# Optimization experiments

Measured on AMD Instinct MI355X. Metric: run time of the kernel, lower is better.

Reference implementation:

```python
import jax, jax.numpy as jnp
import numpy as np

B, T, N, F = 1, 12, 20000, 1
E = 320000
D, H, NH = 64, 64, 4


def setup_inputs() -> dict:
    ki = iter(jax.random.split(jax.random.key(0), 64))

    def rn(shape, s=0.05):
        return jax.random.normal(next(ki), shape, jnp.float32) * s

    z = lambda *s: jnp.zeros(s, jnp.float32)
    o = lambda *s: jnp.ones(s, jnp.float32)
    inp = {}
    inp['x_seq'] = jax.random.normal(next(ki), (B, T, N, F), jnp.float32)
    inp['edge_index'] = jax.random.randint(next(ki), (2, E), 0, N)
    inp['edge_weight'] = jax.random.uniform(next(ki), (E,), jnp.float32)
    inp['Wpi'] = rn((F, D)); inp['bpi'] = z(D)
    for nm, shp in [('Wq', (D, D)), ('Wk', (D, D)), ('Wv', (D, D)), ('Wo', (D, D)), ('W1', (D, 4 * D)), ('W2', (4 * D, D)), ('Wpo', (D, F))]:
        inp[nm] = rn(shp)
    for nm, d in [('bq', D), ('bk', D), ('bv', D), ('bo', D), ('b1', 4 * D), ('b2', D), ('bpo', F)]:
        inp[nm] = z(d)
    inp['g1'] = o(D); inp['be1'] = z(D); inp['g2'] = o(D); inp['be2'] = z(D)
    # GConvGRU gate params: A* (x self), B* (x neighbor), C*/D* (h self/neighbor)
    for a, bn, bb, c, d, cb in [('Az', 'Bz', 'bz', 'Cz', 'Dz', 'cz'), ('Ar', 'Br', 'br', 'Cr', 'Dr', 'cr'), ('Ah', 'Bh', 'bg', 'Ch', 'Dh', 'cg')]:
        inp[a] = rn((F, H)); inp[bn] = rn((F, H)); inp[bb] = z(H)
        inp[c] = rn((H, H)); inp[d] = rn((H, H)); inp[cb] = z(H)
    inp['Whd'] = rn((H, 1)); inp['bhd'] = z(1)
    return inp


def reference(x_seq, edge_index, edge_weight, Wpi, bpi, Wq, bq, Wk, bk, Wv, bv, Wo, bo, g1, be1, W1, b1, W2, b2, g2, be2, Wpo, bpo, Az, Bz, bz, Cz, Dz, cz, Ar, Br, br, Cr, Dr, cr, Ah, Bh, bg, Ch, Dh, cg, Whd, bhd):
    B_, T_, N_, F_ = x_seq.shape
    M = B_ * N_
    dh = D // NH

    def ln(y, g, b):
        m = y.mean(-1, keepdims=True)
        v = ((y - m) ** 2).mean(-1, keepdims=True)
        return (y - m) / jnp.sqrt(v + 1e-5) * g + b

    # per-node temporal Transformer (post-LN, relu FFN, dropout=eval)
    x = x_seq.transpose(0, 2, 1, 3).reshape(M, T_, F_)  # [M,T,F]
    x = x @ Wpi + bpi  # [M,T,D]
    q = (x @ Wq + bq).reshape(M, T_, NH, dh)
    k = (x @ Wk + bk).reshape(M, T_, NH, dh)
    v = (x @ Wv + bv).reshape(M, T_, NH, dh)
    att = jax.nn.softmax(jnp.einsum('mqhd,mkhd->mhqk', q, k) / jnp.sqrt(jnp.float32(dh)), axis=-1)
    a = jnp.einsum('mhqk,mkhd->mqhd', att, v).reshape(M, T_, D) @ Wo + bo
    x = ln(x + a, g1, be1)
    f = jax.nn.relu(x @ W1 + b1) @ W2 + b2
    x = ln(x + f, g2, be2)
    x = x @ Wpo + bpo  # [M,T,F]
    xs = x.reshape(B_, N_, T_, F_).transpose(2, 0, 1, 3)  # [T,B,N,F]

    src, dst = edge_index[0], edge_index[1]
    ew = edge_weight[None, :, None]

    def gconv(y, Ws, Wn, b):
        msg = jnp.zeros_like(y).at[:, dst].add(y[:, src] * ew)
        return y @ Ws + msg @ Wn + b

    def step(h, xt):
        zt = jax.nn.sigmoid(gconv(xt, Az, Bz, bz) + gconv(h, Cz, Dz, cz))
        rt = jax.nn.sigmoid(gconv(xt, Ar, Br, br) + gconv(h, Cr, Dr, cr))
        gt = jnp.tanh(gconv(xt, Ah, Bh, bg) + gconv(rt * h, Ch, Dh, cg))
        h = zt * h + (1.0 - zt) * gt
        return h, None

    h0 = jnp.zeros((B_, N_, H), x_seq.dtype)
    h, _ = jax.lax.scan(step, h0, xs)
    return jax.nn.relu(h) @ Whd + bhd  # [B,N,1]
```

## Files before the change

kernel.cpp:

```cpp
#include <hip/hip_runtime.h>
#include <math.h>

#define TT 12
#define NN 20000
#define EE 320000

__device__ __forceinline__ float wsum64(float v) {
#pragma unroll
    for (int o = 32; o >= 1; o >>= 1) v += __shfl_xor(v, o);
    return v;
}

__device__ __forceinline__ float wsum16(float v) {
#pragma unroll
    for (int o = 8; o >= 1; o >>= 1) v += __shfl_xor(v, o);
    return v;
}

__device__ __forceinline__ float rdlane(float v, int l) {
    return __int_as_float(__builtin_amdgcn_readlane(__float_as_int(v), l));
}

__global__ void k_precomp(const float* __restrict__ Wpi, const float* __restrict__ bpi,
                          const float* __restrict__ Wq, const float* __restrict__ bq,
                          const float* __restrict__ Wk, const float* __restrict__ bk,
                          const float* __restrict__ Wv, const float* __restrict__ bv,
                          const float* __restrict__ Wo, const float* __restrict__ bo,
                          const float* __restrict__ g1, const float* __restrict__ be1,
                          const float* __restrict__ W1, const float* __restrict__ b1,
                          float* __restrict__ PC) {
    __shared__ float sWq[64], sWk[64], sWv[64], sBq[64], sBk[64], sBv[64];
    const int tid = threadIdx.x;
    if (tid < 64) {
        int d = tid;
        float wq = 0, wk = 0, wv = 0, vbq = 0, vbk = 0, vbv = 0;
        for (int e = 0; e < 64; ++e) {
            float wp = Wpi[e], bp = bpi[e];
            wq = fmaf(wp, Wq[e * 64 + d], wq);
            wk = fmaf(wp, Wk[e * 64 + d], wk);
            wv = fmaf(wp, Wv[e * 64 + d], wv);
            vbq = fmaf(bp, Wq[e * 64 + d], vbq);
            vbk = fmaf(bp, Wk[e * 64 + d], vbk);
            vbv = fmaf(bp, Wv[e * 64 + d], vbv);
        }
        sWq[d] = wq; sWk[d] = wk; sWv[d] = wv;
        sBq[d] = vbq + bq[d]; sBk[d] = vbk + bk[d]; sBv[d] = vbv + bv[d];
    }
    __syncthreads();
    if (tid < 16) {
        int h = tid >> 2, which = tid & 3;
        float s = 0;
        for (int j = 0; j < 16; ++j) {
            int e = h * 16 + j;
            float a = (which < 2) ? sWq[e] : sBq[e];
            float b = (which & 1) ? sBk[e] : sWk[e];
            s = fmaf(a, b, s);
        }
        PC[320 + which * 4 + h] = s;
    }
    {
        int h = tid >> 6, d = tid & 63;
        float s = 0;
        for (int j = 0; j < 16; ++j) {
            int e = h * 16 + j;
            s = fmaf(sWv[e], Wo[e * 64 + d], s);
        }
        PC[h * 64 + d] = s;
    }
    if (tid < 64) {
        int d = tid;
        float s = 0;
        for (int e = 0; e < 64; ++e) s = fmaf(sBv[e], Wo[e * 64 + d], s);
        PC[256 + d] = s + bo[d] + bpi[d];
    }
    __syncthreads();
    {
        int k = tid;
        for (int r = 0; r < 8; ++r) {
            float s = (r == 7) ? b1[k] : 0.0f;
            for (int d = 0; d < 64; ++d) {
                float b;
                if (r == 0) b = Wpi[d] * g1[d];
                else if (r < 5) b = PC[(r - 1) * 64 + d] * g1[d];
                else if (r == 5) b = PC[256 + d] * g1[d];
                else if (r == 6) b = g1[d];
                else b = be1[d];
                s = fmaf(b, W1[d * 256 + k], s);
            }
            PC[384 + r * 256 + k] = s;
        }
    }
}

__global__ void k_zero_offs(int* __restrict__ offs) {
    int i = blockIdx.x * 256 + threadIdx.x;
    if (i < NN + 1) offs[i] = 0;
}
__global__ void k_count(const int* __restrict__ dst, int* __restrict__ offs) {
    int e = blockIdx.x * 256 + threadIdx.x;
    if (e < EE) atomicAdd(&offs[dst[e] + 1], 1);
}
__global__ void k_scan(int* __restrict__ offs, int* __restrict__ cur) {
    __shared__ int buf[1024];
    __shared__ int carry;
    int tid = threadIdx.x;
    if (tid == 0) carry = 0;
    __syncthreads();
    const int total = NN + 1;
    for (int base = 0; base < total; base += 1024) {
        int idx = base + tid;
        int v = (idx < total) ? offs[idx] : 0;
        buf[tid] = v;
        __syncthreads();
        for (int o = 1; o < 1024; o <<= 1) {
            int t = (tid >= o) ? buf[tid - o] : 0;
            __syncthreads();
            buf[tid] += t;
            __syncthreads();
        }
        int incl = buf[tid] + carry;
        if (idx < total) offs[idx] = incl;
        __syncthreads();
        if (tid == 1023) carry += buf[1023];
        __syncthreads();
    }
    for (int i = tid; i < NN; i += 1024) cur[i] = offs[i];
}
__global__ void k_fill(const int* __restrict__ src, const int* __restrict__ dst,
                       const float* __restrict__ w, int* __restrict__ cur,
                       int2* __restrict__ ep) {
    int e = blockIdx.x * 256 + threadIdx.x;
    if (e < EE) {
        int dn = dst[e];
        int slot = atomicAdd(&cur[dn], 1);
        ep[slot] = make_int2(src[e], __float_as_int(w[e]));
    }
}

__global__ void __launch_bounds__(256)
k_transformer(const float* __restrict__ x_seq,
              const float* __restrict__ Wpi,
              const float* __restrict__ g1, const float* __restrict__ be1,
              const float* __restrict__ b2,
              const float* __restrict__ g2, const float* __restrict__ be2,
              const float* __restrict__ W2,
              const float* __restrict__ PC,
              const float* __restrict__ Wpo, const float* __restrict__ bpo,
              float* __restrict__ XS) {
    __shared__ __align__(16) float sCV[4][TT][4];
    __shared__ __align__(16) float sRelu[4][TT][64];
    __shared__ __align__(16) float sX1[4][TT][64];
    __shared__ float sIvsv[4][TT];
    __shared__ float sMiv[4][TT];
    const int wid = threadIdx.x >> 6;
    const int d = threadIdx.x & 63;
    const int n = blockIdx.x * 4 + wid;

    float sv[TT];
#pragma unroll
    for (int t = 0; t < TT; ++t) sv[t] = x_seq[t * NN + n];

    {
        const int hh = d >> 4;
        const int qi = d & 15;
        const float alpha = PC[320 + hh], beta = PC[324 + hh];
        const float gamma = PC[328 + hh], delta = PC[332 + hh];
        if (qi < TT) {
            float si = sv[qi];
            float a1 = 0.25f * fmaf(si, alpha, gamma);
            float a0 = 0.25f * fmaf(si, beta, delta);
            float sc[TT];
            float mx = -1e30f;
#pragma unroll
            for (int j = 0; j < TT; ++j) {
                sc[j] = fmaf(sv[j], a1, a0);
                mx = fmaxf(mx, sc[j]);
            }
            float ssum = 0.f;
#pragma unroll
            for (int j = 0; j < TT; ++j) { sc[j] = __expf(sc[j] - mx); ssum += sc[j]; }
            float inv = 1.0f / ssum;
            float cv = 0.f;
#pragma unroll
            for (int j = 0; j < TT; ++j) cv = fmaf(sc[j] * inv, sv[j], cv);
            sCV[wid][qi][hh] = cv;
        }
    }
    __syncthreads();

    float ivv[TT];
    const float inv64 = 1.0f / 64.0f;
    {
        const float u = Wpi[d];
        const float g1d = g1[d], be1d = be1[d];
        const float vo0 = PC[d], vo1 = PC[64 + d], vo2 = PC[128 + d], vo3 = PC[192 + d];
        const float c0 = PC[256 + d];
#pragma unroll
        for (int t = 0; t < TT; ++t) {
            float4 cv4 = *(const float4*)(&sCV[wid][t][0]);
            float y = fmaf(sv[t], u, c0);
            y = fmaf(cv4.x, vo0, y); y = fmaf(cv4.y, vo1, y);
            y = fmaf(cv4.z, vo2, y); y = fmaf(cv4.w, vo3, y);
            float s1 = wsum64(y);
            float s2 = wsum64(y * y);
            float m = s1 * inv64;
            float var = s2 * inv64 - m * m;
            float iv = rsqrtf(var + 1e-5f);
            ivv[t] = iv;
            sX1[wid][t][d] = (y - m) * iv * g1d + be1d;
            if (d == 0) {
                sIvsv[wid][t] = sv[t] * iv;
                sMiv[wid][t] = -m * iv;
            }
        }
    }

    float y2[TT];
    {
        float b2d = b2[d];
#pragma unroll
        for (int t = 0; t < TT; ++t) y2[t] = b2d;
    }
#pragma unroll
    for (int kk = 0; kk < 4; ++kk) {
        const float* P = PC + 384 + kk * 64 + d;
        float P0 = P[0], P1 = P[256], P2 = P[512], P3 = P[768];
        float P4 = P[1024], P5 = P[1280], P6 = P[1536], P7 = P[1792];
#pragma unroll
        for (int t = 0; t < TT; ++t) {
            float4 cv4 = *(const float4*)(&sCV[wid][t][0]);
            float iv = ivv[t];
            float hp = P7;
            hp = fmaf(sIvsv[wid][t], P0, hp);
            hp = fmaf(cv4.x * iv, P1, hp);
            hp = fmaf(cv4.y * iv, P2, hp);
            hp = fmaf(cv4.z * iv, P3, hp);
            hp = fmaf(cv4.w * iv, P4, hp);
            hp = fmaf(iv, P5, hp);
            hp = fmaf(sMiv[wid][t], P6, hp);
            sRelu[wid][t][d] = fmaxf(hp, 0.0f);
        }
#pragma unroll 4
        for (int kg = 0; kg < 64; kg += 4) {
            const float* wb = W2 + (kk * 64 + kg) * 64 + d;
            float w0 = wb[0], w1 = wb[64], w2 = wb[128], w3 = wb[192];
#pragma unroll
            for (int t = 0; t < TT; ++t) {
                float4 rv = *(const float4*)(&sRelu[wid][t][kg]);
                y2[t] = fmaf(rv.x, w0, fmaf(rv.y, w1, fmaf(rv.z, w2, fmaf(rv.w, w3, y2[t]))));
            }
        }
    }

    {
        float g2d = g2[d], be2d = be2[d], wpod = Wpo[d];
        float bpo0 = bpo[0];
#pragma unroll
        for (int t = 0; t < TT; ++t) {
            float y = sX1[wid][t][d] + y2[t];
            float s1 = wsum64(y);
            float s2 = wsum64(y * y);
            float m = s1 * inv64;
            float var = s2 * inv64 - m * m;
            float iv = rsqrtf(var + 1e-5f);
            float x2 = (y - m) * iv * g2d + be2d;
            float p = wsum64(x2 * wpod);
            if (d == 0) XS[n * TT + t] = p + bpo0;
        }
    }
}

__global__ void k_gather_x(const float* __restrict__ XS,
                           const int* __restrict__ offs, const int2* __restrict__ ep,
                           float* __restrict__ MX) {
    const int wid = threadIdx.x >> 6;
    const int lane = threadIdx.x & 63;
    const int lg = lane >> 4;
    const int el = lane & 15;
    const int n = (blockIdx.x * 4 + wid) * 4 + lg;
    int beg = offs[n], end = offs[n + 1];
    float4 a0 = {0,0,0,0}, a1 = {0,0,0,0}, a2 = {0,0,0,0};
    for (int i = beg + el; i < end; i += 16) {
        int2 e = ep[i];
        float w = __int_as_float(e.y);
        const float4* xr = (const float4*)(XS + (size_t)e.x * TT);
        float4 v0 = xr[0], v1 = xr[1], v2 = xr[2];
        a0.x = fmaf(w, v0.x, a0.x); a0.y = fmaf(w, v0.y, a0.y);
        a0.z = fmaf(w, v0.z, a0.z); a0.w = fmaf(w, v0.w, a0.w);
        a1.x = fmaf(w, v1.x, a1.x); a1.y = fmaf(w, v1.y, a1.y);
        a1.z = fmaf(w, v1.z, a1.z); a1.w = fmaf(w, v1.w, a1.w);
        a2.x = fmaf(w, v2.x, a2.x); a2.y = fmaf(w, v2.y, a2.y);
        a2.z = fmaf(w, v2.z, a2.z); a2.w = fmaf(w, v2.w, a2.w);
    }
    float acc[TT] = { a0.x, a0.y, a0.z, a0.w, a1.x, a1.y, a1.z, a1.w,
                      a2.x, a2.y, a2.z, a2.w };
#pragma unroll
    for (int t = 0; t < TT; ++t) acc[t] = wsum16(acc[t]);
    if (el == 0) {
#pragma unroll
        for (int t = 0; t < TT; ++t) MX[n * TT + t] = acc[t];
    }
}

__global__ void k_gather_vec(const float* __restrict__ V,
                             const int* __restrict__ offs, const int2* __restrict__ ep,
                             float* __restrict__ out) {
    const int wid = threadIdx.x >> 6;
    const int d = threadIdx.x & 63;
    const int n = blockIdx.x * 4 + wid;
    int beg = offs[n], end = offs[n + 1];
    float m0 = 0, m1 = 0, m2 = 0, m3 = 0, m4 = 0, m5 = 0, m6 = 0, m7 = 0;
    int i = beg;
    for (; i + 8 <= end; i += 8) {
        int2 e0 = ep[i], e1 = ep[i+1], e2 = ep[i+2], e3 = ep[i+3];
        int2 e4 = ep[i+4], e5 = ep[i+5], e6 = ep[i+6], e7 = ep[i+7];
        m0 = fmaf(__int_as_float(e0.y), V[(size_t)e0.x * 64 + d], m0);
        m1 = fmaf(__int_as_float(e1.y), V[(size_t)e1.x * 64 + d], m1);
        m2 = fmaf(__int_as_float(e2.y), V[(size_t)e2.x * 64 + d], m2);
        m3 = fmaf(__int_as_float(e3.y), V[(size_t)e3.x * 64 + d], m3);
        m4 = fmaf(__int_as_float(e4.y), V[(size_t)e4.x * 64 + d], m4);
        m5 = fmaf(__int_as_float(e5.y), V[(size_t)e5.x * 64 + d], m5);
        m6 = fmaf(__int_as_float(e6.y), V[(size_t)e6.x * 64 + d], m6);
        m7 = fmaf(__int_as_float(e7.y), V[(size_t)e7.x * 64 + d], m7);
    }
    for (; i < end; ++i) {
        int2 e = ep[i];
        m0 = fmaf(__int_as_float(e.y), V[(size_t)e.x * 64 + d], m0);
    }
    out[(size_t)n * 64 + d] = ((m0 + m1) + (m2 + m3)) + ((m4 + m5) + (m6 + m7));
}

__global__ void k_gates_a(const float* __restrict__ XS, const float* __restrict__ MX, int tstep,
                          const float* __restrict__ h, const float* __restrict__ MH,
                          const float* __restrict__ Az, const float* __restrict__ Bz,
                          const float* __restrict__ bz,
                          const float* __restrict__ Cz, const float* __restrict__ Dz,
                          const float* __restrict__ cz,
                          const float* __restrict__ Ar, const float* __restrict__ Br,
                          const float* __restrict__ br,
                          const float* __restrict__ Cr, const float* __restrict__ Dr,
                          const float* __restrict__ cr,
                          float* __restrict__ zb, float* __restrict__ rh) {
    const int wid = threadIdx.x >> 6;
    const int d = threadIdx.x & 63;
    const int nb = (blockIdx.x * 4 + wid) * 8;

    float hreg[8], mreg[8], zacc[8], racc[8];
    {
        float azd = Az[d], bzd = Bz[d], cz0 = bz[d] + cz[d];
        float ard = Ar[d], brd = Br[d], cr0 = br[d] + cr[d];
#pragma unroll
        for (int g = 0; g < 8; ++g) {
            int n = nb + g;
            hreg[g] = h[(size_t)n * 64 + d];
            mreg[g] = MH[(size_t)n * 64 + d];
            float xt = XS[n * TT + tstep];
            float mx = MX[n * TT + tstep];
            zacc[g] = fmaf(xt, azd, fmaf(mx, bzd, cz0));
            racc[g] = fmaf(xt, ard, fmaf(mx, brd, cr0));
        }
    }
#pragma unroll 4
    for (int k = 0; k < 64; ++k) {
        float wcz = Cz[k * 64 + d], wdz = Dz[k * 64 + d];
        float wcr = Cr[k * 64 + d], wdr = Dr[k * 64 + d];
#pragma unroll
        for (int g = 0; g < 8; ++g) {
            float hk = rdlane(hreg[g], k);
            float mk = rdlane(mreg[g], k);
            zacc[g] = fmaf(hk, wcz, fmaf(mk, wdz, zacc[g]));
            racc[g] = fmaf(hk, wcr, fmaf(mk, wdr, racc[g]));
        }
    }
#pragma unroll
    for (int g = 0; g < 8; ++g) {
        int n = nb + g;
        float z = 1.0f / (1.0f + __expf(-zacc[g]));
        float r = 1.0f / (1.0f + __expf(-racc[g]));
        zb[(size_t)n * 64 + d] = z;
        rh[(size_t)n * 64 + d] = r * hreg[g];
    }
}

__global__ void k_gates_b(const float* __restrict__ XS, const float* __restrict__ MX, int tstep,
                          float* __restrict__ h,
                          const float* __restrict__ zb, const float* __restrict__ rh,
                          const float* __restrict__ MRH,
                          const float* __restrict__ Ah, const float* __restrict__ Bh,
                          const float* __restrict__ bg,
                          const float* __restrict__ Ch, const float* __restrict__ Dh,
                          const float* __restrict__ cg,
                          const float* __restrict__ Whd, const float* __restrict__ bhd,
                          float* __restrict__ out, int last) {
    const int wid = threadIdx.x >> 6;
    const int d = threadIdx.x & 63;
    const int nb = (blockIdx.x * 4 + wid) * 8;

    float rreg[8], mreg[8], gacc[8];
    {
        float ahd = Ah[d], bhd_ = Bh[d], cg0 = bg[d] + cg[d];
#pragma unroll
        for (int g = 0; g < 8; ++g) {
            int n = nb + g;
            rreg[g] = rh[(size_t)n * 64 + d];
            mreg[g] = MRH[(size_t)n * 64 + d];
            float xt = XS[n * TT + tstep];
            float mx = MX[n * TT + tstep];
            gacc[g] = fmaf(xt, ahd, fmaf(mx, bhd_, cg0));
        }
    }
#pragma unroll 4
    for (int k = 0; k < 64; ++k) {
        float wch = Ch[k * 64 + d], wdh = Dh[k * 64 + d];
#pragma unroll
        for (int g = 0; g < 8; ++g) {
            float rk = rdlane(rreg[g], k);
            float mk = rdlane(mreg[g], k);
            gacc[g] = fmaf(rk, wch, fmaf(mk, wdh, gacc[g]));
        }
    }
#pragma unroll
    for (int g = 0; g < 8; ++g) {
        int n = nb + g;
        float gg = tanhf(gacc[g]);
        float z = zb[(size_t)n * 64 + d];
        float hold = h[(size_t)n * 64 + d];
        float hnew = z * hold + (1.0f - z) * gg;
        h[(size_t)n * 64 + d] = hnew;
        if (last) {
            float p = fmaxf(hnew, 0.0f) * Whd[d];
            float s = wsum64(p);
            if (d == 0) out[n] = s + bhd[0];
        }
    }
}

extern "C" void kernel_launch(void* const* d_in, const int* in_sizes, int n_in,
                              void* d_out, int out_size, void* d_ws, size_t ws_size,
                              hipStream_t stream) {
    const float* x_seq = (const float*)d_in[0];
    const int* eidx = (const int*)d_in[1];
    const float* ew = (const float*)d_in[2];
    const float* Wpi = (const float*)d_in[3];
    const float* bpi = (const float*)d_in[4];
    const float* Wq = (const float*)d_in[5];
    const float* Wk = (const float*)d_in[6];
    const float* Wv = (const float*)d_in[7];
    const float* Wo = (const float*)d_in[8];
    const float* W1 = (const float*)d_in[9];
    const float* W2 = (const float*)d_in[10];
    const float* Wpo = (const float*)d_in[11];
    const float* bq = (const float*)d_in[12];
    const float* bk = (const float*)d_in[13];
    const float* bv = (const float*)d_in[14];
    const float* bo = (const float*)d_in[15];
    const float* b1 = (const float*)d_in[16];
    const float* b2 = (const float*)d_in[17];
    const float* bpo = (const float*)d_in[18];
    const float* g1 = (const float*)d_in[19];
    const float* be1 = (const float*)d_in[20];
    const float* g2 = (const float*)d_in[21];
    const float* be2 = (const float*)d_in[22];
    const float* Az = (const float*)d_in[23];
    const float* Bz = (const float*)d_in[24];
    const float* bz = (const float*)d_in[25];
    const float* Cz = (const float*)d_in[26];
    const float* Dz = (const float*)d_in[27];
    const float* cz = (const float*)d_in[28];
    const float* Ar = (const float*)d_in[29];
    const float* Br = (const float*)d_in[30];
    const float* br_ = (const float*)d_in[31];
    const float* Cr = (const float*)d_in[32];
    const float* Dr = (const float*)d_in[33];
    const float* cr_ = (const float*)d_in[34];
    const float* Ah = (const float*)d_in[35];
    const float* Bh = (const float*)d_in[36];
    const float* bg = (const float*)d_in[37];
    const float* Ch = (const float*)d_in[38];
    const float* Dh = (const float*)d_in[39];
    const float* cg = (const float*)d_in[40];
    const float* Whd = (const float*)d_in[41];
    const float* bhd = (const float*)d_in[42];

    float* ws = (float*)d_ws;
    float* XS = ws;
    float* hbuf = XS + 240000;
    float* rhbuf = hbuf + 1280000;
    float* zbuf = rhbuf + 1280000;
    float* msg = zbuf + 1280000;
    float* PC = msg + 1280000;
    int* ioffs = (int*)(PC + 2560);
    int* cur = ioffs + (NN + 1);
    int2* ep = (int2*)(cur + NN + 1);
    float* MX = (float*)(ep + EE);

    const int* e_src = eidx;
    const int* e_dst = eidx + EE;

    hipMemsetAsync(hbuf, 0, (size_t)NN * 64 * sizeof(float), stream);
    k_precomp<<<1, 256, 0, stream>>>(Wpi, bpi, Wq, bq, Wk, bk, Wv, bv, Wo, bo,
                                     g1, be1, W1, b1, PC);
    k_zero_offs<<<(NN + 1 + 255) / 256, 256, 0, stream>>>(ioffs);
    k_count<<<(EE + 255) / 256, 256, 0, stream>>>(e_dst, ioffs);
    k_scan<<<1, 1024, 0, stream>>>(ioffs, cur);
    k_fill<<<(EE + 255) / 256, 256, 0, stream>>>(e_src, e_dst, ew, cur, ep);

    k_transformer<<<5000, 256, 0, stream>>>(x_seq, Wpi, g1, be1, b2, g2, be2,
                                            W2, PC, Wpo, bpo, XS);

    k_gather_x<<<1250, 256, 0, stream>>>(XS, ioffs, ep, MX);

    for (int t = 0; t < TT; ++t) {
        k_gather_vec<<<5000, 256, 0, stream>>>(hbuf, ioffs, ep, msg);
        k_gates_a<<<625, 256, 0, stream>>>(XS, MX, t, hbuf, msg,
                                           Az, Bz, bz, Cz, Dz, cz,
                                           Ar, Br, br_, Cr, Dr, cr_,
                                           zbuf, rhbuf);
        k_gather_vec<<<5000, 256, 0, stream>>>(rhbuf, ioffs, ep, msg);
        k_gates_b<<<625, 256, 0, stream>>>(XS, MX, t, hbuf, zbuf, rhbuf, msg,
                                           Ah, Bh, bg, Ch, Dh, cg,
                                           Whd, bhd, (float*)d_out, (t == TT - 1) ? 1 : 0);
    }
}
```

Before: 1.376 ms.

## Fuse GRU time loop into one cooperative kernel; keep FFN hidden in registers

The 48 per-timestep launches of the GRU recurrence are replaced by a single persistent cooperative kernel. It runs the gather and gate phases with grid-wide syncs between them, with the multi-launch path kept as a fallback. Separately, the transformer FFN now holds the ReLU hidden activations in registers and broadcasts them with readlane instead of staging them in shared memory. The aim is to remove launch overhead and shared-memory traffic. The trade-offs are grid.sync cost, a grid size limited by occupancy, and higher register pressure in the transformer (launch bounds set to 1).

```diff
diff --git a/kernel.cpp b/kernel.cpp
--- a/kernel.cpp
+++ b/kernel.cpp
@@ -1,5 +1,8 @@
 #include <hip/hip_runtime.h>
+#include <hip/hip_cooperative_groups.h>
 #include <math.h>
+
+namespace cg = cooperative_groups;
 
 #define TT 12
 #define NN 20000
@@ -137,7 +140,7 @@
     }
 }
 
-__global__ void __launch_bounds__(256)
+__global__ void __launch_bounds__(256, 1)
 k_transformer(const float* __restrict__ x_seq,
               const float* __restrict__ Wpi,
               const float* __restrict__ g1, const float* __restrict__ be1,
@@ -148,7 +151,6 @@
               const float* __restrict__ Wpo, const float* __restrict__ bpo,
               float* __restrict__ XS) {
     __shared__ __align__(16) float sCV[4][TT][4];
-    __shared__ __align__(16) float sRelu[4][TT][64];
     __shared__ __align__(16) float sX1[4][TT][64];
     __shared__ float sIvsv[4][TT];
     __shared__ float sMiv[4][TT];
@@ -214,41 +216,51 @@
             }
         }
     }
-
-    float y2[TT];
-    {
-        float b2d = b2[d];
-#pragma unroll
-        for (int t = 0; t < TT; ++t) y2[t] = b2d;
-    }
-#pragma unroll
-    for (int kk = 0; kk < 4; ++kk) {
-        const float* P = PC + 384 + kk * 64 + d;
-        float P0 = P[0], P1 = P[256], P2 = P[512], P3 = P[768];
-        float P4 = P[1024], P5 = P[1280], P6 = P[1536], P7 = P[1792];
+    __syncthreads();
+
+    float hpreg[TT][4];
+    {
+        float Pr[8][4];
+#pragma unroll
+        for (int r = 0; r < 8; ++r)
+#pragma unroll
+            for (int kk = 0; kk < 4; ++kk)
+                Pr[r][kk] = PC[384 + r * 256 + kk * 64 + d];
 #pragma unroll
         for (int t = 0; t < TT; ++t) {
             float4 cv4 = *(const float4*)(&sCV[wid][t][0]);
             float iv = ivv[t];
-            float hp = P7;
-            hp = fmaf(sIvsv[wid][t], P0, hp);
-            hp = fmaf(cv4.x * iv, P1, hp);
-            hp = fmaf(cv4.y * iv, P2, hp);
-            hp = fmaf(cv4.z * iv, P3, hp);
-            hp = fmaf(cv4.w * iv, P4, hp);
-            hp = fmaf(iv, P5, hp);
-            hp = fmaf(sMiv[wid][t], P6, hp);
-            sRelu[wid][t][d] = fmaxf(hp, 0.0f);
-        }
+            float civ = sIvsv[wid][t];
+            float cmv = sMiv[wid][t];
+#pragma unroll
+            for (int kk = 0; kk < 4; ++kk) {
+                float hp = Pr[7][kk];
+                hp = fmaf(civ, Pr[0][kk], hp);
+                hp = fmaf(cv4.x * iv, Pr[1][kk], hp);
+                hp = fmaf(cv4.y * iv, Pr[2][kk], hp);
+                hp = fmaf(cv4.z * iv, Pr[3][kk], hp);
+                hp = fmaf(cv4.w * iv, Pr[4][kk], hp);
+                hp = fmaf(iv, Pr[5][kk], hp);
+                hp = fmaf(cmv, Pr[6][kk], hp);
+                hpreg[t][kk] = fmaxf(hp, 0.0f);
+            }
+        }
+    }
+
+    float y2[TT];
+    {
+        float b2d = b2[d];
+#pragma unroll
+        for (int t = 0; t < TT; ++t) y2[t] = b2d;
+    }
+#pragma unroll
+    for (int kk = 0; kk < 4; ++kk) {
 #pragma unroll 4
-        for (int kg = 0; kg < 64; kg += 4) {
-            const float* wb = W2 + (kk * 64 + kg) * 64 + d;
-            float w0 = wb[0], w1 = wb[64], w2 = wb[128], w3 = wb[192];
-#pragma unroll
-            for (int t = 0; t < TT; ++t) {
-                float4 rv = *(const float4*)(&sRelu[wid][t][kg]);
-                y2[t] = fmaf(rv.x, w0, fmaf(rv.y, w1, fmaf(rv.z, w2, fmaf(rv.w, w3, y2[t]))));
-            }
+        for (int kin = 0; kin < 64; ++kin) {
+            float w = W2[(kk * 64 + kin) * 64 + d];
+#pragma unroll
+            for (int t = 0; t < TT; ++t)
+                y2[t] = fmaf(rdlane(hpreg[t][kk], kin), w, y2[t]);
         }
     }
 
@@ -432,6 +444,164 @@
             float s = wsum64(p);
             if (d == 0) out[n] = s + bhd[0];
         }
+    }
+}
+
+__global__ void __launch_bounds__(256, 4)
+k_gru_coop(const float* __restrict__ XS, const float* __restrict__ MX,
+           float* __restrict__ h, float* __restrict__ zb, float* __restrict__ rh,
+           float* __restrict__ msg,
+           const int* __restrict__ offs, const int2* __restrict__ ep,
+           const float* __restrict__ Az, const float* __restrict__ Bz,
+           const float* __restrict__ bz,
+           const float* __restrict__ Cz, const float* __restrict__ Dz,
+           const float* __restrict__ cz,
+           const float* __restrict__ Ar, const float* __restrict__ Br,
+           const float* __restrict__ br,
+           const float* __restrict__ Cr, const float* __restrict__ Dr,
+           const float* __restrict__ cr,
+           const float* __restrict__ Ah, const float* __restrict__ Bh,
+           const float* __restrict__ bg,
+           const float* __restrict__ Ch, const float* __restrict__ Dh,
+           const float* __restrict__ cg,
+           const float* __restrict__ Whd, const float* __restrict__ bhd,
+           float* __restrict__ out) {
+    cg::grid_group grid = cg::this_grid();
+    const int wid = threadIdx.x >> 6;
+    const int d = threadIdx.x & 63;
+    const int gw = blockIdx.x * 4 + wid;
+    const int NW = gridDim.x * 4;
+
+    for (int t = 0; t < TT; ++t) {
+        for (int n = gw; n < NN; n += NW) {
+            int beg = offs[n], end = offs[n + 1];
+            float m0 = 0, m1 = 0, m2 = 0, m3 = 0, m4 = 0, m5 = 0, m6 = 0, m7 = 0;
+            int i = beg;
+            for (; i + 8 <= end; i += 8) {
+                int2 e0 = ep[i], e1 = ep[i+1], e2 = ep[i+2], e3 = ep[i+3];
+                int2 e4 = ep[i+4], e5 = ep[i+5], e6 = ep[i+6], e7 = ep[i+7];
+                m0 = fmaf(__int_as_float(e0.y), h[(size_t)e0.x * 64 + d], m0);
+                m1 = fmaf(__int_as_float(e1.y), h[(size_t)e1.x * 64 + d], m1);
+                m2 = fmaf(__int_as_float(e2.y), h[(size_t)e2.x * 64 + d], m2);
+                m3 = fmaf(__int_as_float(e3.y), h[(size_t)e3.x * 64 + d], m3);
+                m4 = fmaf(__int_as_float(e4.y), h[(size_t)e4.x * 64 + d], m4);
+                m5 = fmaf(__int_as_float(e5.y), h[(size_t)e5.x * 64 + d], m5);
+                m6 = fmaf(__int_as_float(e6.y), h[(size_t)e6.x * 64 + d], m6);
+                m7 = fmaf(__int_as_float(e7.y), h[(size_t)e7.x * 64 + d], m7);
+            }
+            for (; i < end; ++i) {
+                int2 e = ep[i];
+                m0 = fmaf(__int_as_float(e.y), h[(size_t)e.x * 64 + d], m0);
+            }
+            msg[(size_t)n * 64 + d] = ((m0 + m1) + (m2 + m3)) + ((m4 + m5) + (m6 + m7));
+        }
+        grid.sync();
+
+        for (int task = gw; task < NN / 8; task += NW) {
+            const int nb = task * 8;
+            float hreg[8], mreg[8], zacc[8], racc[8];
+            {
+                float azd = Az[d], bzd = Bz[d], cz0 = bz[d] + cz[d];
+                float ard = Ar[d], brd = Br[d], cr0 = br[d] + cr[d];
+#pragma unroll
+                for (int g = 0; g < 8; ++g) {
+                    int n = nb + g;
+                    hreg[g] = h[(size_t)n * 64 + d];
+                    mreg[g] = msg[(size_t)n * 64 + d];
+                    float xt = XS[n * TT + t];
+                    float mx = MX[n * TT + t];
+                    zacc[g] = fmaf(xt, azd, fmaf(mx, bzd, cz0));
+                    racc[g] = fmaf(xt, ard, fmaf(mx, brd, cr0));
+                }
+            }
+#pragma unroll 4
+            for (int k = 0; k < 64; ++k) {
+                float wcz = Cz[k * 64 + d], wdz = Dz[k * 64 + d];
+                float wcr = Cr[k * 64 + d], wdr = Dr[k * 64 + d];
+#pragma unroll
+                for (int g = 0; g < 8; ++g) {
+                    float hk = rdlane(hreg[g], k);
+                    float mk = rdlane(mreg[g], k);
+                    zacc[g] = fmaf(hk, wcz, fmaf(mk, wdz, zacc[g]));
+                    racc[g] = fmaf(hk, wcr, fmaf(mk, wdr, racc[g]));
+                }
+            }
+#pragma unroll
+            for (int g = 0; g < 8; ++g) {
+                int n = nb + g;
+                float z = 1.0f / (1.0f + __expf(-zacc[g]));
+                float r = 1.0f / (1.0f + __expf(-racc[g]));
+                zb[(size_t)n * 64 + d] = z;
+                rh[(size_t)n * 64 + d] = r * hreg[g];
+            }
+        }
+        grid.sync();
+
+        for (int n = gw; n < NN; n += NW) {
+            int beg = offs[n], end = offs[n + 1];
+            float m0 = 0, m1 = 0, m2 = 0, m3 = 0, m4 = 0, m5 = 0, m6 = 0, m7 = 0;
+            int i = beg;
+            for (; i + 8 <= end; i += 8) {
+                int2 e0 = ep[i], e1 = ep[i+1], e2 = ep[i+2], e3 = ep[i+3];
+                int2 e4 = ep[i+4], e5 = ep[i+5], e6 = ep[i+6], e7 = ep[i+7];
+                m0 = fmaf(__int_as_float(e0.y), rh[(size_t)e0.x * 64 + d], m0);
+                m1 = fmaf(__int_as_float(e1.y), rh[(size_t)e1.x * 64 + d], m1);
+                m2 = fmaf(__int_as_float(e2.y), rh[(size_t)e2.x * 64 + d], m2);
+                m3 = fmaf(__int_as_float(e3.y), rh[(size_t)e3.x * 64 + d], m3);
+                m4 = fmaf(__int_as_float(e4.y), rh[(size_t)e4.x * 64 + d], m4);
+                m5 = fmaf(__int_as_float(e5.y), rh[(size_t)e5.x * 64 + d], m5);
+                m6 = fmaf(__int_as_float(e6.y), rh[(size_t)e6.x * 64 + d], m6);
+                m7 = fmaf(__int_as_float(e7.y), rh[(size_t)e7.x * 64 + d], m7);
+            }
+            for (; i < end; ++i) {
+                int2 e = ep[i];
+                m0 = fmaf(__int_as_float(e.y), rh[(size_t)e.x * 64 + d], m0);
+            }
+            msg[(size_t)n * 64 + d] = ((m0 + m1) + (m2 + m3)) + ((m4 + m5) + (m6 + m7));
+        }
+        grid.sync();
+
+        for (int task = gw; task < NN / 8; task += NW) {
+            const int nb = task * 8;
+            float rreg[8], mreg[8], gacc[8];
+            {
+                float ahd = Ah[d], bhd_ = Bh[d], cg0 = bg[d] + cg[d];
+#pragma unroll
+                for (int g = 0; g < 8; ++g) {
+                    int n = nb + g;
+                    rreg[g] = rh[(size_t)n * 64 + d];
+                    mreg[g] = msg[(size_t)n * 64 + d];
+                    float xt = XS[n * TT + t];
+                    float mx = MX[n * TT + t];
+                    gacc[g] = fmaf(xt, ahd, fmaf(mx, bhd_, cg0));
+                }
+            }
+#pragma unroll 4
+            for (int k = 0; k < 64; ++k) {
+                float wch = Ch[k * 64 + d], wdh = Dh[k * 64 + d];
+#pragma unroll
+                for (int g = 0; g < 8; ++g) {
+                    float rk = rdlane(rreg[g], k);
+                    float mk = rdlane(mreg[g], k);
+                    gacc[g] = fmaf(rk, wch, fmaf(mk, wdh, gacc[g]));
+                }
+            }
+#pragma unroll
+            for (int g = 0; g < 8; ++g) {
+                int n = nb + g;
+                float gg = tanhf(gacc[g]);
+                float z = zb[(size_t)n * 64 + d];
+                float hold = h[(size_t)n * 64 + d];
+                float hnew = z * hold + (1.0f - z) * gg;
+                h[(size_t)n * 64 + d] = hnew;
+                if (t == TT - 1) {
+                    float p = fmaxf(hnew, 0.0f) * Whd[d];
+                    float s = wsum64(p);
+                    if (d == 0) out[n] = s + bhd[0];
+                }
+            }
+        }
+        grid.sync();
     }
 }
 
@@ -497,7 +667,7 @@
     const int* e_src = eidx;
     const int* e_dst = eidx + EE;
 
-    hipMemsetAsync(hbuf, 0, (size_t)NN * 64 * sizeof(float), stream);
+    (void)hipMemsetAsync(hbuf, 0, (size_t)NN * 64 * sizeof(float), stream);
     k_precomp<<<1, 256, 0, stream>>>(Wpi, bpi, Wq, bq, Wk, bk, Wv, bv, Wo, bo,
                                      g1, be1, W1, b1, PC);
     k_zero_offs<<<(NN + 1 + 255) / 256, 256, 0, stream>>>(ioffs);
@@ -510,15 +680,37 @@
 
     k_gather_x<<<1250, 256, 0, stream>>>(XS, ioffs, ep, MX);
 
-    for (int t = 0; t < TT; ++t) {
-        k_gather_vec<<<5000, 256, 0, stream>>>(hbuf, ioffs, ep, msg);
-        k_gates_a<<<625, 256, 0, stream>>>(XS, MX, t, hbuf, msg,
-                                           Az, Bz, bz, Cz, Dz, cz,
-                                           Ar, Br, br_, Cr, Dr, cr_,
-                                           zbuf, rhbuf);
-        k_gather_vec<<<5000, 256, 0, stream>>>(rhbuf, ioffs, ep, msg);
-        k_gates_b<<<625, 256, 0, stream>>>(XS, MX, t, hbuf, zbuf, rhbuf, msg,
-                                           Ah, Bh, bg, Ch, Dh, cg,
-                                           Whd, bhd, (float*)d_out, (t == TT - 1) ? 1 : 0);
-    }
-}
+    bool coop_done = false;
+    {
+        int maxPerCU = 0;
+        hipError_t qe = hipOccupancyMaxActiveBlocksPerMultiprocessor(&maxPerCU, k_gru_coop, 256, 0);
+        int nblk = (qe == hipSuccess && maxPerCU > 0) ? maxPerCU * 256 : 512;
+        if (nblk > 2048) nblk = 2048;
+        float* out = (float*)d_out;
+        void* args[] = {
+            (void*)&XS, (void*)&MX, (void*)&hbuf, (void*)&zbuf, (void*)&rhbuf,
+            (void*)&msg, (void*)&ioffs, (void*)&ep,
+            (void*)&Az, (void*)&Bz, (void*)&bz, (void*)&Cz, (void*)&Dz, (void*)&cz,
+            (void*)&Ar, (void*)&Br, (void*)&br_, (void*)&Cr, (void*)&Dr, (void*)&cr_,
+            (void*)&Ah, (void*)&Bh, (void*)&bg, (void*)&Ch, (void*)&Dh, (void*)&cg,
+            (void*)&Whd, (void*)&bhd, (void*)&out
+        };
+        if (hipLaunchCooperativeKernel((void*)k_gru_coop, dim3(nblk), dim3(256),
+                                       args, 0, stream) == hipSuccess) {
+            coop_done = true;
+        }
+    }
+    if (!coop_done) {
+        for (int t = 0; t < TT; ++t) {
+            k_gather_vec<<<5000, 256, 0, stream>>>(hbuf, ioffs, ep, msg);
+            k_gates_a<<<625, 256, 0, stream>>>(XS, MX, t, hbuf, msg,
+                                               Az, Bz, bz, Cz, Dz, cz,
+                                               Ar, Br, br_, Cr, Dr, cr_,
+                                               zbuf, rhbuf);
+            k_gather_vec<<<5000, 256, 0, stream>>>(rhbuf, ioffs, ep, msg);
+            k_gates_b<<<625, 256, 0, stream>>>(XS, MX, t, hbuf, zbuf, rhbuf, msg,
+                                               Ah, Bh, bg, Ch, Dh, cg,
+                                               Whd, bhd, (float*)d_out, (t == TT - 1) ? 1 : 0);
+        }
+    }
+}
```

Measured after the change: 4.888 ms. 3.55x slower.
